# Optimization experiments

Hardware: AMD Instinct MI355X
Metric: run time of the kernel (lower is better)

The kernel has to match this reference:

```python
import jax, jax.numpy as jnp
import numpy as np

T, OBS, HID, OUT = 8192, 256, 2048, 256
IN_SIZE = 2 * OBS  # ys concatenated with its NaN mask


def setup_inputs() -> dict:
    key = jax.random.key(0)
    ks = jax.random.split(key, 7)
    s_i = 1.0 / np.sqrt(IN_SIZE)
    s_h = 1.0 / np.sqrt(HID)
    return {
        "ts": jnp.arange(T, dtype=jnp.float32),
        "ys": jax.random.normal(ks[0], (T, OBS), jnp.float32),
        "wi": jax.random.normal(ks[1], (3 * HID, IN_SIZE), jnp.float32) * s_i,
        "wh": jax.random.normal(ks[2], (3 * HID, HID), jnp.float32) * s_h,
        "b": jax.random.normal(ks[3], (3 * HID,), jnp.float32) * s_h,
        "bn": jax.random.normal(ks[4], (HID,), jnp.float32) * s_h,
        "Wl": jax.random.normal(ks[5], (OUT, HID), jnp.float32) * s_h,
        "bl": jax.random.normal(ks[6], (OUT,), jnp.float32) * s_h,
    }


def _gru_forward(ys, wi, wh, b, bn, Wl, bl):
    # NaN-mask preprocessing, as in the module's __call__.
    mask = (~jnp.isnan(ys)).astype(ys.dtype)          # [T, OBS]
    x = jnp.concatenate([jnp.nan_to_num(ys), mask], axis=-1)  # [T, 2*OBS]

    # Precompute all input-to-hidden gate projections in one big GEMM
    # (mathematically identical to doing wi @ x_t inside the scan).
    igates = x @ wi.T + b                             # [T, 3H]

    def step(h, ig):
        hg = wh @ h                                   # [3H]
        ir, iz, ig_n = jnp.split(ig, 3)
        hr, hz, hn = jnp.split(hg, 3)
        r = jax.nn.sigmoid(ir + hr)                   # reset gate
        z = jax.nn.sigmoid(iz + hz)                   # update gate (eqx 'inp')
        n = jnp.tanh(ig_n + r * (hn + bn))            # candidate
        h_new = n + z * (h - n)                       # eqx GRUCell output
        return h_new, h_new

    h0 = jnp.zeros((wh.shape[1],), ys.dtype)
    _, hidden_ts = jax.lax.scan(step, h0, igates)     # [T, H]

    # evolving_out=True: apply the linear head at every timestep.
    return hidden_ts @ Wl.T + bl                      # [T, OUT]


def reference(ts, ys, wi, wh, b, bn, Wl, bl):
    # ts is unused when including_dts=False, matching the module.
    return _gru_forward(ys, wi, wh, b, bn, Wl, bl)
```

## Files before the change

### kernel.cpp

```cpp
#include <hip/hip_runtime.h>
#include <hip/hip_bf16.h>

#define T_STEPS 8192
#define OBS 256
#define HID 2048
#define NOUT 256

#define NBLK 128
#define NTHR 512
#define NSLOT 512

typedef unsigned long long u64;
typedef _Float16 half2v __attribute__((ext_vector_type(2)));
typedef __fp16 fp16x2 __attribute__((ext_vector_type(2)));

#define WS_HBUF_OFF 4096
#define WS_HIDDEN_OFF 65536

__global__ void gru_init_kernel(u64* h_pair) {
  h_pair[blockIdx.x * 256 + threadIdx.x] = 0ull;
}

__device__ __forceinline__ half2v bc_h2(unsigned u) {
  union { unsigned u; half2v h; } c;
  c.u = u;
  return c.h;
}
__device__ __forceinline__ unsigned pk_rn(float lo, float hi) {
  union { half2v h; unsigned u; } c;
  c.h[0] = (_Float16)lo;
  c.h[1] = (_Float16)hi;
  return c.u;
}
__device__ __forceinline__ unsigned pk_rtz(float lo, float hi) {
  union { fp16x2 h; unsigned u; } c;
  c.h = __builtin_amdgcn_cvt_pkrtz(lo, hi);
  return c.u;
}
__device__ __forceinline__ float fdot2f(unsigned a, unsigned b, float c) {
#if __has_builtin(__builtin_amdgcn_fdot2)
  return __builtin_amdgcn_fdot2(bc_h2(a), bc_h2(b), c, false);
#else
  const half2v ha = bc_h2(a), hb = bc_h2(b);
  return c + (float)ha[0] * (float)hb[0] + (float)ha[1] * (float)hb[1];
#endif
}

__global__ __launch_bounds__(NTHR, 2) void gru_scan_kernel(
    const float* __restrict__ ys, const float* __restrict__ wi,
    const float* __restrict__ wh, const float* __restrict__ b,
    const float* __restrict__ bn, __hip_bfloat16* __restrict__ hidden,
    u64* h_pair) {
  const int w = blockIdx.x;
  const int tid = threadIdx.x;
  const int wave = tid >> 6;
  const int lane = tid & 63;

  __shared__ __align__(16) unsigned hq_lds[2][HID / 2];
  __shared__ unsigned pair_lds[2][8];

  unsigned whp[6][16];
  unsigned wip[6][4];
#pragma unroll
  for (int r = 0; r < 6; ++r) {
    const int g = r >> 1, e = r & 1;
    const size_t R = (size_t)(g * HID + w * 16 + 2 * wave + e);
#pragma unroll
    for (int m = 0; m < 8; ++m) {
      const float4 q =
          *reinterpret_cast<const float4*>(wh + R * HID + m * 256 + lane * 4);
      whp[r][2 * m] = pk_rn(q.x, q.y);
      whp[r][2 * m + 1] = pk_rn(q.z, q.w);
    }
#pragma unroll
    for (int p = 0; p < 2; ++p) {
      const float4 q =
          *reinterpret_cast<const float4*>(wi + R * 512 + p * 256 + lane * 4);
      wip[r][2 * p] = pk_rn(q.x, q.y);
      wip[r][2 * p + 1] = pk_rn(q.z, q.w);
    }
  }
#pragma unroll
  for (int r = 0; r < 6; ++r) {
#pragma unroll
    for (int m = 0; m < 16; ++m) asm volatile("" : "+v"(whp[r][m]));
#pragma unroll
    for (int p = 0; p < 4; ++p) asm volatile("" : "+v"(wip[r][p]));
  }

  const int iu = w * 16 + 2 * wave + (lane & 1);
  const float b_r = b[iu];
  const float b_z = b[HID + iu];
  const float b_n = b[2 * HID + iu];
  const float bn_v = bn[iu];

  float h_own = 0.f;

#pragma unroll 1
  for (int s = 0; s < T_STEPS; ++s) {
    const int buf = s & 1;
    const u64* hp = h_pair + buf * (2 * NSLOT);
    u64* hp_next = h_pair + (buf ^ 1) * (2 * NSLOT);
    const unsigned tag = (unsigned)s;

    u64 v0 = __hip_atomic_load(hp + 2 * tid, __ATOMIC_RELAXED,
                               __HIP_MEMORY_SCOPE_AGENT);
    u64 v1 = __hip_atomic_load(hp + 2 * tid + 1, __ATOMIC_RELAXED,
                               __HIP_MEMORY_SCOPE_AGENT);

    const float4 yv =
        *reinterpret_cast<const float4*>(ys + (size_t)s * OBS + lane * 4);
    const bool k0 = (yv.x == yv.x), k1 = (yv.y == yv.y), k2 = (yv.z == yv.z),
               k3 = (yv.w == yv.w);
    unsigned xq[4];
    xq[0] = pk_rtz(k0 ? yv.x : 0.f, k1 ? yv.y : 0.f);
    xq[1] = pk_rtz(k2 ? yv.z : 0.f, k3 ? yv.w : 0.f);
    xq[2] = pk_rtz(k0 ? 1.f : 0.f, k1 ? 1.f : 0.f);
    xq[3] = pk_rtz(k2 ? 1.f : 0.f, k3 ? 1.f : 0.f);

    float pR[2], pZ[2], pIN[2];
#pragma unroll
    for (int e = 0; e < 2; ++e) {
      float ar = 0.f, az = 0.f, ain = 0.f;
#pragma unroll
      for (int p = 0; p < 4; ++p) {
        ar = fdot2f(wip[e][p], xq[p], ar);
        az = fdot2f(wip[2 + e][p], xq[p], az);
        ain = fdot2f(wip[4 + e][p], xq[p], ain);
      }
      pR[e] = ar;
      pZ[e] = az;
      pIN[e] = ain;
    }

    while ((unsigned)(v0 >> 32) != tag || (unsigned)v1 != tag) {
      __builtin_amdgcn_s_sleep(1);
      v0 = __hip_atomic_load(hp + 2 * tid, __ATOMIC_RELAXED,
                             __HIP_MEMORY_SCOPE_AGENT);
      v1 = __hip_atomic_load(hp + 2 * tid + 1, __ATOMIC_RELAXED,
                             __HIP_MEMORY_SCOPE_AGENT);
    }

    hq_lds[buf][2 * tid] = (unsigned)v0;
    hq_lds[buf][2 * tid + 1] = (unsigned)(v1 >> 32);
    __syncthreads();

    unsigned hq[16];
#pragma unroll
    for (int m = 0; m < 8; ++m) {
      const uint2 q =
          *reinterpret_cast<const uint2*>(&hq_lds[buf][m * 128 + lane * 2]);
      hq[2 * m] = q.x;
      hq[2 * m + 1] = q.y;
    }

    float a[8];
#pragma unroll
    for (int e = 0; e < 2; ++e) {
      float ar = pR[e], az = pZ[e], ahn = 0.f;
      const int r0 = e, r1 = 2 + e, r2 = 4 + e;
#pragma unroll
      for (int m = 0; m < 16; ++m) {
        ar = fdot2f(whp[r0][m], hq[m], ar);
        az = fdot2f(whp[r1][m], hq[m], az);
        ahn = fdot2f(whp[r2][m], hq[m], ahn);
      }
      a[4 * e] = ar;
      a[4 * e + 1] = az;
      a[4 * e + 2] = ahn;
      a[4 * e + 3] = pIN[e];
    }

#pragma unroll
    for (int j = 0; j < 4; ++j) {
      const bool sel = (lane & 1) != 0;
      const float keep = sel ? a[j + 4] : a[j];
      const float send = sel ? a[j] : a[j + 4];
      a[j] = keep + __shfl_xor(send, 1, 64);
    }
#pragma unroll
    for (int j = 0; j < 2; ++j) {
      const bool sel = (lane & 2) != 0;
      const float keep = sel ? a[j + 2] : a[j];
      const float send = sel ? a[j] : a[j + 2];
      a[j] = keep + __shfl_xor(send, 2, 64);
    }
    {
      const bool sel = (lane & 4) != 0;
      const float keep = sel ? a[1] : a[0];
      const float send = sel ? a[0] : a[1];
      a[0] = keep + __shfl_xor(send, 4, 64);
    }
    float redv = a[0];
    redv += __shfl_xor(redv, 8, 64);
    redv += __shfl_xor(redv, 16, 64);
    redv += __shfl_xor(redv, 32, 64);

    const int e = lane & 1;
    const float d_r = __shfl(redv, e, 64);
    const float d_z = __shfl(redv, 4 + e, 64);
    const float d_hn = __shfl(redv, 2 + e, 64);
    const float d_in = __shfl(redv, 6 + e, 64);

    const float rg = 1.f / (1.f + expf(-(d_r + b_r)));
    const float zg = 1.f / (1.f + expf(-(d_z + b_z)));
    const float ng = tanhf(d_in + b_n + rg * (d_hn + bn_v));
    const float hnew = ng + zg * (h_own - ng);
    h_own = hnew;

    const float h1 = __shfl(hnew, 1, 64);
    if (lane == 0) {
      pair_lds[buf][wave] = pk_rtz(hnew, h1);
      const unsigned bf =
          ((unsigned)__bfloat16_as_ushort(__float2bfloat16(h1)) << 16) |
          (unsigned)__bfloat16_as_ushort(__float2bfloat16(hnew));
      *reinterpret_cast<unsigned*>(
          &hidden[(size_t)s * HID + w * 16 + 2 * wave]) = bf;
    }
    __syncthreads();

    if (tid < 8) {
      const int q = tid >> 1;
      u64 pv;
      if ((tid & 1) == 0)
        pv = ((u64)(tag + 1) << 32) | (u64)pair_lds[buf][2 * q];
      else
        pv = ((u64)pair_lds[buf][2 * q + 1] << 32) | (u64)(tag + 1);
      __hip_atomic_store(hp_next + w * 8 + tid, pv, __ATOMIC_RELAXED,
                         __HIP_MEMORY_SCOPE_AGENT);
    }
  }
}

__global__ __launch_bounds__(256) void out_gemm_kernel(
    const __hip_bfloat16* __restrict__ hidden, const float* __restrict__ Wl,
    const float* __restrict__ bl, float* __restrict__ out) {
  __shared__ float As[16][68];
  __shared__ float Bs[16][68];
  const int tid = threadIdx.x;
  const int bt = blockIdx.x * 64;
  const int bo = blockIdx.y * 64;
  const int tx = tid & 15;
  const int ty = tid >> 4;
  const int tA = tid >> 2;
  const int kq = (tid & 3) << 2;
  const unsigned short* hidu = reinterpret_cast<const unsigned short*>(hidden);

  float acc[4][4];
#pragma unroll
  for (int i = 0; i < 4; ++i)
#pragma unroll
    for (int j = 0; j < 4; ++j) acc[i][j] = 0.f;

  for (int k0 = 0; k0 < HID; k0 += 16) {
    const ushort4 av = *reinterpret_cast<const ushort4*>(
        hidu + (size_t)(bt + tA) * HID + k0 + kq);
    As[kq + 0][tA] = __uint_as_float((unsigned)av.x << 16);
    As[kq + 1][tA] = __uint_as_float((unsigned)av.y << 16);
    As[kq + 2][tA] = __uint_as_float((unsigned)av.z << 16);
    As[kq + 3][tA] = __uint_as_float((unsigned)av.w << 16);
    const float4 bv = *reinterpret_cast<const float4*>(
        Wl + (size_t)(bo + tA) * HID + k0 + kq);
    Bs[kq + 0][tA] = bv.x;
    Bs[kq + 1][tA] = bv.y;
    Bs[kq + 2][tA] = bv.z;
    Bs[kq + 3][tA] = bv.w;
    __syncthreads();
#pragma unroll
    for (int k = 0; k < 16; ++k) {
      const float4 a = *reinterpret_cast<const float4*>(&As[k][ty << 2]);
      const float4 bq = *reinterpret_cast<const float4*>(&Bs[k][tx << 2]);
      const float a4[4] = {a.x, a.y, a.z, a.w};
      const float b4[4] = {bq.x, bq.y, bq.z, bq.w};
#pragma unroll
      for (int i = 0; i < 4; ++i)
#pragma unroll
        for (int j = 0; j < 4; ++j) acc[i][j] += a4[i] * b4[j];
    }
    __syncthreads();
  }
#pragma unroll
  for (int i = 0; i < 4; ++i) {
    const int t = bt + (ty << 2) + i;
#pragma unroll
    for (int j = 0; j < 4; ++j) {
      const int o = bo + (tx << 2) + j;
      out[(size_t)t * NOUT + o] = acc[i][j] + bl[o];
    }
  }
}

extern "C" void kernel_launch(void* const* d_in, const int* in_sizes, int n_in,
                              void* d_out, int out_size, void* d_ws,
                              size_t ws_size, hipStream_t stream) {
  (void)in_sizes;
  (void)n_in;
  (void)out_size;
  (void)ws_size;
  const float* ys = (const float*)d_in[1];
  const float* wi = (const float*)d_in[2];
  const float* wh = (const float*)d_in[3];
  const float* b = (const float*)d_in[4];
  const float* bn = (const float*)d_in[5];
  const float* Wl = (const float*)d_in[6];
  const float* bl = (const float*)d_in[7];
  float* out = (float*)d_out;

  u64* h_pair = (u64*)((char*)d_ws + WS_HBUF_OFF);
  __hip_bfloat16* hidden = (__hip_bfloat16*)((char*)d_ws + WS_HIDDEN_OFF);

  gru_init_kernel<<<8, 256, 0, stream>>>(h_pair);

  gru_scan_kernel<<<dim3(NBLK), dim3(NTHR), 0, stream>>>(ys, wi, wh, b, bn,
                                                         hidden, h_pair);

  out_gemm_kernel<<<dim3(T_STEPS / 64, NOUT / 64), 256, 0, stream>>>(
      hidden, Wl, bl, out);
}
```

Before: 20.85 ms.

## Publish per-wave hidden slots directly, dropping the second block barrier

Each wave's lane 0 now writes its own tagged 64-bit slot (fp16 pair plus step tag) straight to global memory. Before, waves staged their results in LDS and a second __syncthreads let 8 threads publish them. The slots are padded to a 32-byte stride, live in the output buffer (overwritten later by the GEMM), and pollers only reload slots that are still stale. This removes one block-wide barrier per step from the critical path of the recurrence, at the cost of more strided slot traffic and reuse of the output buffer as scratch.

```diff
diff --git a/kernel.cpp b/kernel.cpp
--- a/kernel.cpp
+++ b/kernel.cpp
@@ -8,17 +8,16 @@
 
 #define NBLK 128
 #define NTHR 512
-#define NSLOT 512
 
 typedef unsigned long long u64;
 typedef _Float16 half2v __attribute__((ext_vector_type(2)));
 typedef __fp16 fp16x2 __attribute__((ext_vector_type(2)));
 
-#define WS_HBUF_OFF 4096
 #define WS_HIDDEN_OFF 65536
-
-__global__ void gru_init_kernel(u64* h_pair) {
-  h_pair[blockIdx.x * 256 + threadIdx.x] = 0ull;
+#define SLOT_STRIDE 4
+
+__global__ void gru_init_kernel(u64* slots) {
+  slots[blockIdx.x * 256 + threadIdx.x] = 0ull;
 }
 
 __device__ __forceinline__ half2v bc_h2(unsigned u) {
@@ -50,14 +49,13 @@
     const float* __restrict__ ys, const float* __restrict__ wi,
     const float* __restrict__ wh, const float* __restrict__ b,
     const float* __restrict__ bn, __hip_bfloat16* __restrict__ hidden,
-    u64* h_pair) {
+    u64* slots) {
   const int w = blockIdx.x;
   const int tid = threadIdx.x;
   const int wave = tid >> 6;
   const int lane = tid & 63;
 
   __shared__ __align__(16) unsigned hq_lds[2][HID / 2];
-  __shared__ unsigned pair_lds[2][8];
 
   unsigned whp[6][16];
   unsigned wip[6][4];
@@ -99,14 +97,14 @@
 #pragma unroll 1
   for (int s = 0; s < T_STEPS; ++s) {
     const int buf = s & 1;
-    const u64* hp = h_pair + buf * (2 * NSLOT);
-    u64* hp_next = h_pair + (buf ^ 1) * (2 * NSLOT);
+    const u64* hp = slots + buf * (1024 * SLOT_STRIDE);
+    u64* hp_next = slots + (buf ^ 1) * (1024 * SLOT_STRIDE);
     const unsigned tag = (unsigned)s;
 
-    u64 v0 = __hip_atomic_load(hp + 2 * tid, __ATOMIC_RELAXED,
+    u64 v0 = __hip_atomic_load(hp + (2 * tid) * SLOT_STRIDE, __ATOMIC_RELAXED,
                                __HIP_MEMORY_SCOPE_AGENT);
-    u64 v1 = __hip_atomic_load(hp + 2 * tid + 1, __ATOMIC_RELAXED,
-                               __HIP_MEMORY_SCOPE_AGENT);
+    u64 v1 = __hip_atomic_load(hp + (2 * tid + 1) * SLOT_STRIDE,
+                               __ATOMIC_RELAXED, __HIP_MEMORY_SCOPE_AGENT);
 
     const float4 yv =
         *reinterpret_cast<const float4*>(ys + (size_t)s * OBS + lane * 4);
@@ -133,16 +131,18 @@
       pIN[e] = ain;
     }
 
-    while ((unsigned)(v0 >> 32) != tag || (unsigned)v1 != tag) {
+    while ((unsigned)(v0 >> 32) != tag || (unsigned)(v1 >> 32) != tag) {
       __builtin_amdgcn_s_sleep(1);
-      v0 = __hip_atomic_load(hp + 2 * tid, __ATOMIC_RELAXED,
-                             __HIP_MEMORY_SCOPE_AGENT);
-      v1 = __hip_atomic_load(hp + 2 * tid + 1, __ATOMIC_RELAXED,
-                             __HIP_MEMORY_SCOPE_AGENT);
+      if ((unsigned)(v0 >> 32) != tag)
+        v0 = __hip_atomic_load(hp + (2 * tid) * SLOT_STRIDE, __ATOMIC_RELAXED,
+                               __HIP_MEMORY_SCOPE_AGENT);
+      if ((unsigned)(v1 >> 32) != tag)
+        v1 = __hip_atomic_load(hp + (2 * tid + 1) * SLOT_STRIDE,
+                               __ATOMIC_RELAXED, __HIP_MEMORY_SCOPE_AGENT);
     }
 
     hq_lds[buf][2 * tid] = (unsigned)v0;
-    hq_lds[buf][2 * tid + 1] = (unsigned)(v1 >> 32);
+    hq_lds[buf][2 * tid + 1] = (unsigned)v1;
     __syncthreads();
 
     unsigned hq[16];
@@ -210,24 +210,14 @@
 
     const float h1 = __shfl(hnew, 1, 64);
     if (lane == 0) {
-      pair_lds[buf][wave] = pk_rtz(hnew, h1);
+      const u64 pv = ((u64)(tag + 1) << 32) | (u64)pk_rtz(hnew, h1);
+      __hip_atomic_store(hp_next + (w * 8 + wave) * SLOT_STRIDE, pv,
+                         __ATOMIC_RELAXED, __HIP_MEMORY_SCOPE_AGENT);
       const unsigned bf =
           ((unsigned)__bfloat16_as_ushort(__float2bfloat16(h1)) << 16) |
           (unsigned)__bfloat16_as_ushort(__float2bfloat16(hnew));
       *reinterpret_cast<unsigned*>(
           &hidden[(size_t)s * HID + w * 16 + 2 * wave]) = bf;
-    }
-    __syncthreads();
-
-    if (tid < 8) {
-      const int q = tid >> 1;
-      u64 pv;
-      if ((tid & 1) == 0)
-        pv = ((u64)(tag + 1) << 32) | (u64)pair_lds[buf][2 * q];
-      else
-        pv = ((u64)pair_lds[buf][2 * q + 1] << 32) | (u64)(tag + 1);
-      __hip_atomic_store(hp_next + w * 8 + tid, pv, __ATOMIC_RELAXED,
-                         __HIP_MEMORY_SCOPE_AGENT);
     }
   }
 }
@@ -306,13 +296,13 @@
   const float* bl = (const float*)d_in[7];
   float* out = (float*)d_out;
 
-  u64* h_pair = (u64*)((char*)d_ws + WS_HBUF_OFF);
+  u64* slots = (u64*)d_out;
   __hip_bfloat16* hidden = (__hip_bfloat16*)((char*)d_ws + WS_HIDDEN_OFF);
 
-  gru_init_kernel<<<8, 256, 0, stream>>>(h_pair);
+  gru_init_kernel<<<32, 256, 0, stream>>>(slots);
 
   gru_scan_kernel<<<dim3(NBLK), dim3(NTHR), 0, stream>>>(ys, wi, wh, b, bn,
-                                                         hidden, h_pair);
+                                                         hidden, slots);
 
   out_gemm_kernel<<<dim3(T_STEPS / 64, NOUT / 64), 256, 0, stream>>>(
       hidden, Wl, bl, out);
```

Result: slower. 30.76 ms, median of 2 (+47.5%).
